# Performance work log

Hardware: AMD Instinct MI355X
Metric: run time of the kernel (lower is better)

Reference implementation:

```python
import jax, jax.numpy as jnp
import numpy as np

N = 50000
E = 1600000
HID = 128
H = 8
D = HID // H


def _layer_norm(x, g, b, eps=1e-5):
    mu = jnp.mean(x, axis=-1, keepdims=True)
    var = jnp.mean(jnp.square(x - mu), axis=-1, keepdims=True)
    return (x - mu) * jax.lax.rsqrt(var + eps) * g + b


def setup_inputs() -> dict:
    key = jax.random.key(0)
    ks = jax.random.split(key, 20)
    s = 1.0 / np.sqrt(HID)
    inp = {
        "x": jax.random.normal(ks[0], (N, HID), jnp.float32),
        "edge_index": jax.random.randint(ks[1], (2, E), 0, N, jnp.int64),
        "edge_attr": jax.random.randint(ks[2], (E,), 0, 13, jnp.int64),
        # projections (stored as [in, out] so y = x @ W + b)
        "Wq": jax.random.normal(ks[3], (HID, HID), jnp.float32) * s,
        "bq": jnp.zeros((HID,), jnp.float32),
        "Wk": jax.random.normal(ks[4], (HID, HID), jnp.float32) * s,
        "bk": jnp.zeros((HID,), jnp.float32),
        "Wv": jax.random.normal(ks[5], (HID, HID), jnp.float32) * s,
        "bv": jnp.zeros((HID,), jnp.float32),
        "Wo": jax.random.normal(ks[6], (HID, HID), jnp.float32) * s,
        "bo": jnp.zeros((HID,), jnp.float32),
        "edge_bias_table": jax.random.normal(ks[7], (13, H), jnp.float32) * 0.02,
        "W1": jax.random.normal(ks[8], (HID, 4 * HID), jnp.float32) * s,
        "b1": jnp.zeros((4 * HID,), jnp.float32),
        "W2": jax.random.normal(ks[9], (4 * HID, HID), jnp.float32) * (0.5 * s),
        "b2": jnp.zeros((HID,), jnp.float32),
        "g1": jnp.ones((HID,), jnp.float32),
        "be1": jnp.zeros((HID,), jnp.float32),
        "g2": jnp.ones((HID,), jnp.float32),
        "be2": jnp.zeros((HID,), jnp.float32),
    }
    return inp


def reference(x, edge_index, edge_attr, Wq, bq, Wk, bk, Wv, bv, Wo, bo,
              edge_bias_table, W1, b1, W2, b2, g1, be1, g2, be2):
    n = x.shape[0]
    residual = x
    h = _layer_norm(x, g1, be1)
    Q = (h @ Wq + bq).reshape(n, H, D)
    K = (h @ Wk + bk).reshape(n, H, D)
    V = (h @ Wv + bv).reshape(n, H, D)
    src, dst = edge_index[0], edge_index[1]
    # per-edge scores [E, H]
    scores = jnp.sum(Q[dst] * K[src], axis=-1) / np.sqrt(D)
    scores = scores + edge_bias_table[jnp.clip(edge_attr, 0, 12)]
    # scatter softmax over incoming edges of each dst (global max, as in source)
    scores_exp = jnp.exp(scores - jnp.max(scores))
    attn_sum = jax.ops.segment_sum(scores_exp, dst, num_segments=n)  # [N, H]
    attn_w = scores_exp / (attn_sum[dst] + 1e-8)                      # [E, H]
    messages = V[src] * attn_w[..., None]                             # [E, H, D]
    out = jax.ops.segment_sum(messages, dst, num_segments=n)          # [N, H, D]
    out = out.reshape(n, HID) @ Wo + bo
    x = residual + out  # dropout is identity in eval
    residual = x
    h2 = _layer_norm(x, g2, be2)
    ffn = jax.nn.relu(h2 @ W1 + b1) @ W2 + b2
    return residual + ffn
```

## Files before the change

### kernel.cpp

```cpp
#include <hip/hip_runtime.h>
#include <hip/hip_bf16.h>

#define N_NODES 50000
#define E_EDGES 1600000
#define HID 128
#define NH 8
#define HD 16

#define NBKT 196
#define BKT_CAP 9216
#define CHUNK_A 4096
#define EPT 16
#define BINA_BLOCKS ((E_EDGES + CHUNK_A - 1) / CHUNK_A)
#define WCVT_BLOCKS 771
#define LN_BLOCKS 12500
#define QKV_XBLOCKS ((N_NODES + 127) / 128)
#define ATTN_BLOCKS 2048

using short8 = __attribute__((ext_vector_type(8))) short;
using f32x4  = __attribute__((ext_vector_type(4))) float;
using f32x2  = __attribute__((ext_vector_type(2))) float;
typedef _Float16 h16x2 __attribute__((ext_vector_type(2)));

#if defined(__has_builtin) && __has_builtin(__builtin_amdgcn_fdot2)
#define FDOT2(a, b, c) __builtin_amdgcn_fdot2((a), (b), (c), false)
#else
__device__ __forceinline__ float FDOT2(h16x2 a, h16x2 b, float c) {
    return fmaf((float)a[0], (float)b[0], fmaf((float)a[1], (float)b[1], c));
}
#endif

__device__ __forceinline__ float wave_reduce_sum(float v) {
    #pragma unroll
    for (int off = 32; off > 0; off >>= 1) v += __shfl_xor(v, off, 64);
    return v;
}

__device__ __forceinline__ unsigned int packbf2(float a, float b) {
    __hip_bfloat162 t;
    t.x = __float2bfloat16(a);
    t.y = __float2bfloat16(b);
    unsigned int u;
    __builtin_memcpy(&u, &t, 4);
    return u;
}

__device__ __forceinline__ unsigned short bf16u(float v) {
    __hip_bfloat16 t = __float2bfloat16(v);
    unsigned short u;
    __builtin_memcpy(&u, &t, 2);
    return u;
}

__device__ __forceinline__ unsigned char fp8e(float v) {
    return (unsigned char)(__builtin_amdgcn_cvt_pk_fp8_f32(v, v, 0u, false) & 0xFFu);
}

union U4H {
    uint4 u;
    h16x2 h[4];
};

struct KV {
    U4H k0, k1;
    uint4 v;
};

__device__ __forceinline__ KV loadkv(const char* khs, const unsigned char* v8s, unsigned pk) {
    KV r;
    unsigned rr = pk & 0xFFFFu;
    r.k0.u = *(const uint4*)(khs + (rr << 8));
    r.k1.u = *(const uint4*)(khs + (rr << 8) + 16u);
    r.v = *(const uint4*)(v8s + (rr << 7));
    return r;
}

__device__ __forceinline__ void consume_kv(const KV& kv, unsigned pk, bool vd,
                                           const U4H& q0, const U4H& q1,
                                           const float* bLDS, int sub,
                                           f32x2* acc2, float& wsum) {
    float p = 0.f;
    #pragma unroll
    for (int j = 0; j < 4; ++j) p = FDOT2(q0.h[j], kv.k0.h[j], p);
    #pragma unroll
    for (int j = 0; j < 4; ++j) p = FDOT2(q1.h[j], kv.k1.h[j], p);
    float s = p + bLDS[((pk >> 16) & 0xFu) * 8 + sub];
    float w = vd ? __expf(s) : 0.f;
    wsum += w;
    f32x2 w2; w2[0] = w; w2[1] = w;
    f32x2 t;
    t = __builtin_amdgcn_cvt_pk_f32_fp8(kv.v.x, false); acc2[0] = t * w2 + acc2[0];
    t = __builtin_amdgcn_cvt_pk_f32_fp8(kv.v.x, true);  acc2[1] = t * w2 + acc2[1];
    t = __builtin_amdgcn_cvt_pk_f32_fp8(kv.v.y, false); acc2[2] = t * w2 + acc2[2];
    t = __builtin_amdgcn_cvt_pk_f32_fp8(kv.v.y, true);  acc2[3] = t * w2 + acc2[3];
    t = __builtin_amdgcn_cvt_pk_f32_fp8(kv.v.z, false); acc2[4] = t * w2 + acc2[4];
    t = __builtin_amdgcn_cvt_pk_f32_fp8(kv.v.z, true);  acc2[5] = t * w2 + acc2[5];
    t = __builtin_amdgcn_cvt_pk_f32_fp8(kv.v.w, false); acc2[6] = t * w2 + acc2[6];
    t = __builtin_amdgcn_cvt_pk_f32_fp8(kv.v.w, true);  acc2[7] = t * w2 + acc2[7];
}

__global__ __launch_bounds__(256) void prep_kernel(
    const int* __restrict__ ei, const int* __restrict__ attr,
    int* __restrict__ bcur, unsigned int* __restrict__ temp,
    const float* __restrict__ Wq, const float* __restrict__ Wk,
    const float* __restrict__ Wv, const float* __restrict__ Wo,
    const float* __restrict__ W1, const float* __restrict__ W2,
    const float* __restrict__ bq, const float* __restrict__ bk,
    const float* __restrict__ bv,
    __hip_bfloat16* __restrict__ Wqkvt, __hip_bfloat16* __restrict__ Wot,
    __hip_bfloat16* __restrict__ W1t, __hip_bfloat16* __restrict__ W2t,
    float* __restrict__ bqkv,
    const float* __restrict__ x, const float* __restrict__ g1,
    const float* __restrict__ be1, __hip_bfloat16* __restrict__ h_out) {
    __shared__ unsigned int sval[CHUNK_A];
    __shared__ unsigned short sbkt[CHUNK_A];
    __shared__ int hist[NBKT];
    __shared__ int lofs[NBKT];
    __shared__ int gbase[NBKT];
    __shared__ int lcur[NBKT];
    __shared__ int sc[256];
    const int b = blockIdx.x;
    const int tid = threadIdx.x;
    if (b < BINA_BLOCKS) {
        const int e0 = b * CHUNK_A;
        const int n = min(CHUNK_A, E_EDGES - e0);
        for (int i = tid; i < NBKT; i += 256) hist[i] = 0;
        __syncthreads();
        unsigned int v[EPT];
        short bk_[EPT];
        #pragma unroll
        for (int j = 0; j < EPT; ++j) {
            int i = tid + j * 256;
            bk_[j] = -1;
            v[j] = 0;
            if (i < n) {
                int e = e0 + i;
                int src = ei[e];
                int dst = ei[E_EDGES + e];
                int a = attr[e]; a = min(max(a, 0), 12);
                v[j] = (unsigned)src | ((unsigned)a << 16) | ((unsigned)(dst & 255) << 20);
                int bb = dst >> 8;
                bk_[j] = (short)bb;
                atomicAdd(&hist[bb], 1);
            }
        }
        __syncthreads();
        sc[tid] = (tid < NBKT) ? hist[tid] : 0;
        __syncthreads();
        for (int off = 1; off < 256; off <<= 1) {
            int xx = (tid >= off) ? sc[tid - off] : 0;
            __syncthreads();
            sc[tid] += xx;
            __syncthreads();
        }
        if (tid < NBKT) {
            int h = hist[tid];
            lofs[tid] = sc[tid] - h;
            lcur[tid] = 0;
            gbase[tid] = h ? atomicAdd(&bcur[tid], h) : 0;
        }
        __syncthreads();
        #pragma unroll
        for (int j = 0; j < EPT; ++j) {
            if (bk_[j] >= 0) {
                int p = lofs[bk_[j]] + atomicAdd(&lcur[bk_[j]], 1);
                sval[p] = v[j];
                sbkt[p] = (unsigned short)bk_[j];
            }
        }
        __syncthreads();
        for (int i = tid; i < n; i += 256) {
            int bb = sbkt[i];
            temp[(size_t)bb * BKT_CAP + gbase[bb] + (i - lofs[bb])] = sval[i];
        }
    } else if (b < BINA_BLOCKS + WCVT_BLOCKS) {
        int t = (b - BINA_BLOCKS) * 256 + tid;
        if (t >= 196608) {
            int i = t - 196608;
            if (i < 384) bqkv[i] = i < 128 ? bq[i] : (i < 256 ? bk[i - 128] : bv[i - 256]);
            return;
        }
        const float* W; __hip_bfloat16* Wt; int K, N, idx;
        if (t < 65536) {
            int which = t >> 14; idx = t & 16383; K = 128; N = 128;
            W = which == 0 ? Wq : which == 1 ? Wk : which == 2 ? Wv : Wo;
            Wt = which == 3 ? Wot : Wqkvt + which * 16384;
        } else if (t < 131072) { idx = t - 65536;  K = 128; N = 512; W = W1; Wt = W1t; }
        else                   { idx = t - 131072; K = 512; N = 128; W = W2; Wt = W2t; }
        int n = idx / K, k = idx - n * K;
        Wt[idx] = __float2bfloat16(W[(size_t)k * N + n]);
    } else {
        int wave = tid >> 6;
        int lane = tid & 63;
        int row = (b - BINA_BLOCKS - WCVT_BLOCKS) * 4 + wave;
        if (row >= N_NODES) return;
        float2 v = ((const float2*)(x + (size_t)row * HID))[lane];
        float s = wave_reduce_sum(v.x + v.y);
        float mu = s * (1.0f / HID);
        float dx = v.x - mu, dy = v.y - mu;
        float q = wave_reduce_sum(dx * dx + dy * dy);
        float rstd = rsqrtf(q * (1.0f / HID) + 1e-5f);
        float2 gg = ((const float2*)g1)[lane];
        float2 bb = ((const float2*)be1)[lane];
        __hip_bfloat162 o;
        o.x = __float2bfloat16(dx * rstd * gg.x + bb.x);
        o.y = __float2bfloat16(dy * rstd * gg.y + bb.y);
        ((__hip_bfloat162*)(h_out + (size_t)row * HID))[lane] = o;
    }
}

__global__ __launch_bounds__(512) void qkv_binb_kernel(
    const int* __restrict__ bcur, const unsigned int* __restrict__ temp,
    unsigned int* __restrict__ packed, int* __restrict__ offs,
    const __hip_bfloat16* __restrict__ A, const __hip_bfloat16* __restrict__ Wt,
    const float* __restrict__ bias,
    _Float16* __restrict__ Chh, unsigned char* __restrict__ C8, int M) {
    __shared__ short8 smem[2048 + 2048];
    const int tid = threadIdx.x;
    if (blockIdx.x < NBKT) {
        int* cnts = (int*)smem;
        int* hist = cnts + 256;
        int* cur = hist + 256;
        const int b = blockIdx.x;
        if (tid < 256) {
            cnts[tid] = (tid < NBKT) ? bcur[tid] : 0;
            hist[tid] = 0;
        }
        __syncthreads();
        for (int off = 1; off < 256; off <<= 1) {
            int x = 0;
            if (tid < 256 && tid >= off) x = cnts[tid - off];
            __syncthreads();
            if (tid < 256) cnts[tid] += x;
            __syncthreads();
        }
        const int cnt = bcur[b];
        const int start = cnts[b] - cnt;
        const size_t base = (size_t)b * BKT_CAP;
        for (int i = tid; i < cnt; i += 512)
            atomicAdd(&hist[(temp[base + i] >> 20) & 255], 1);
        __syncthreads();
        if (tid < 256) cur[tid] = hist[tid];
        __syncthreads();
        for (int off = 1; off < 256; off <<= 1) {
            int x = 0;
            if (tid < 256 && tid >= off) x = cur[tid - off];
            __syncthreads();
            if (tid < 256) cur[tid] += x;
            __syncthreads();
        }
        const int node0 = b * 256;
        if (tid < 256) {
            int excl = cur[tid] - hist[tid];
            cur[tid] = excl;
            int node = node0 + tid;
            if (node < N_NODES) offs[node] = start + excl;
        }
        if (b == NBKT - 1 && tid == 0) offs[N_NODES] = start + cnt;
        __syncthreads();
        for (int i = tid; i < cnt; i += 512) {
            unsigned int v = temp[base + i];
            int d = (v >> 20) & 255;
            int p = start + atomicAdd(&cur[d], 1);
            packed[p] = v & 0xFFFFFu;
        }
        return;
    }
    const int gb = blockIdx.x - NBKT;
    const int plane = gb / QKV_XBLOCKS;
    const int xb = gb - plane * QKV_XBLOCKS;
    const int row0 = xb * 128;
    const int col0 = plane * 128;
    const int w = tid >> 6, l = tid & 63;
    const int lr = l & 15, hi = l >> 4;
    f32x4 acc[8] = {};
    #pragma unroll
    for (int it = 0; it < 4; ++it) {
        unsigned d = tid + it * 512;
        int r = d >> 4, sd = d & 15;
        int ss = sd ^ (r & 7);
        int gr = row0 + r; if (gr >= M) gr = M - 1;
        __builtin_amdgcn_global_load_lds(
            (const __attribute__((address_space(1))) void*)(A + (size_t)gr * 128 + ss * 8),
            (__attribute__((address_space(3))) void*)(smem + (d & ~63u)),
            16, 0, 0);
    }
    #pragma unroll
    for (int it = 0; it < 4; ++it) {
        unsigned d = tid + it * 512;
        int r = d >> 4, sd = d & 15;
        int ss = sd ^ (r & 7);
        __builtin_amdgcn_global_load_lds(
            (const __attribute__((address_space(1))) void*)(Wt + (size_t)(col0 + r) * 128 + ss * 8),
            (__attribute__((address_space(3))) void*)(smem + 2048 + (d & ~63u)),
            16, 0, 0);
    }
    __syncthreads();
    const int ar = w * 16 + lr;
    #pragma unroll
    for (int ks = 0; ks < 4; ++ks) {
        int s = ks * 4 + hi;
        short8 a = smem[ar * 16 + (s ^ (ar & 7))];
        #pragma unroll
        for (int f = 0; f < 8; ++f) {
            int br = f * 16 + lr;
            short8 b = smem[2048 + br * 16 + (s ^ (br & 7))];
            acc[f] = __builtin_amdgcn_mfma_f32_16x16x32_bf16(a, b, acc[f], 0, 0, 0);
        }
    }
    const float scl = (plane == 0) ? 0.25f : 1.0f;
    #pragma unroll
    for (int f = 0; f < 8; ++f) {
        int c = col0 + f * 16 + lr;
        float bv = bias[c];
        #pragma unroll
        for (int j = 0; j < 4; ++j) {
            int r = row0 + w * 16 + hi * 4 + j;
            if (r < M) {
                float v = acc[f][j] + bv;
                if (plane < 2)
                    Chh[(size_t)plane * N_NODES * 128 + (size_t)r * 128 + (c & 127)] =
                        (_Float16)(v * scl);
                else
                    C8[(size_t)r * 128 + (c & 127)] = fp8e(v);
            }
        }
    }
}

__global__ __launch_bounds__(512) void wo_ln2_kernel(const __hip_bfloat16* __restrict__ A,
                                                     const __hip_bfloat16* __restrict__ Wt,
                                                     const float* __restrict__ bias,
                                                     const float* __restrict__ res,
                                                     __hip_bfloat16* __restrict__ Cb,
                                                     __hip_bfloat16* __restrict__ Cx,
                                                     const float* __restrict__ gw,
                                                     const float* __restrict__ bw,
                                                     int M) {
    __shared__ short8 smem[2048 + 2048];
    const int row0 = blockIdx.x * 128;
    const int tid = threadIdx.x;
    const int w = tid >> 6, l = tid & 63;
    const int lr = l & 15, hi = l >> 4;
    f32x4 acc[8] = {};
    #pragma unroll
    for (int it = 0; it < 4; ++it) {
        unsigned d = tid + it * 512;
        int r = d >> 4, sd = d & 15;
        int ss = sd ^ (r & 7);
        int gr = row0 + r; if (gr >= M) gr = M - 1;
        __builtin_amdgcn_global_load_lds(
            (const __attribute__((address_space(1))) void*)(A + (size_t)gr * 128 + ss * 8),
            (__attribute__((address_space(3))) void*)(smem + (d & ~63u)),
            16, 0, 0);
    }
    #pragma unroll
    for (int it = 0; it < 4; ++it) {
        unsigned d = tid + it * 512;
        int r = d >> 4, sd = d & 15;
        int ss = sd ^ (r & 7);
        __builtin_amdgcn_global_load_lds(
            (const __attribute__((address_space(1))) void*)(Wt + (size_t)r * 128 + ss * 8),
            (__attribute__((address_space(3))) void*)(smem + 2048 + (d & ~63u)),
            16, 0, 0);
    }
    __syncthreads();
    const int ar = w * 16 + lr;
    #pragma unroll
    for (int ks = 0; ks < 4; ++ks) {
        int s = ks * 4 + hi;
        short8 a = smem[ar * 16 + (s ^ (ar & 7))];
        #pragma unroll
        for (int f = 0; f < 8; ++f) {
            int br = f * 16 + lr;
            short8 b = smem[2048 + br * 16 + (s ^ (br & 7))];
            acc[f] = __builtin_amdgcn_mfma_f32_16x16x32_bf16(a, b, acc[f], 0, 0, 0);
        }
    }
    float vv[8][4];
    float gc[8], bc[8];
    #pragma unroll
    for (int f = 0; f < 8; ++f) {
        int c = f * 16 + lr;
        gc[f] = gw[c]; bc[f] = bw[c];
        float bv = bias[c];
        #pragma unroll
        for (int j = 0; j < 4; ++j) {
            int r = row0 + w * 16 + hi * 4 + j;
            int rr = r < M ? r : M - 1;
            vv[f][j] = acc[f][j] + bv + res[(size_t)rr * 128 + c];
        }
    }
    #pragma unroll
    for (int j = 0; j < 4; ++j) {
        int r = row0 + w * 16 + hi * 4 + j;
        float s = 0.f, qq = 0.f;
        #pragma unroll
        for (int f = 0; f < 8; ++f) { s += vv[f][j]; qq += vv[f][j] * vv[f][j]; }
        #pragma unroll
        for (int m = 1; m <= 8; m <<= 1) { s += __shfl_xor(s, m); qq += __shfl_xor(qq, m); }
        float mu = s * (1.0f / 128.0f);
        float rstd = rsqrtf(qq * (1.0f / 128.0f) - mu * mu + 1e-5f);
        if (r < M) {
            #pragma unroll
            for (int f = 0; f < 8; ++f) {
                int c = f * 16 + lr;
                Cx[(size_t)r * 128 + c] = __float2bfloat16(vv[f][j]);
                Cb[(size_t)r * 128 + c] = __float2bfloat16((vv[f][j] - mu) * rstd * gc[f] + bc[f]);
            }
        }
    }
}

__global__ __launch_bounds__(256) void ffn_fused_kernel(
    const __hip_bfloat16* __restrict__ h2,
    const __hip_bfloat16* __restrict__ W1t,
    const float* __restrict__ b1,
    const __hip_bfloat16* __restrict__ W2t,
    const float* __restrict__ b2,
    const __hip_bfloat16* __restrict__ x1b,
    float* __restrict__ outp, int M) {
    __shared__ short8 aLDS[512];
    __shared__ short8 bLDS[1024];
    __shared__ unsigned short fLDS[32 * 512];
    const int tid = threadIdx.x;
    const int row0 = blockIdx.x * 32;
    const int w = tid >> 6, l = tid & 63;
    const int lr = l & 15, hi = l >> 4;
    const int rt = w & 1, ch = w >> 1;
    #pragma unroll
    for (int it = 0; it < 2; ++it) {
        unsigned d = tid + it * 256;
        int r = d >> 4, sd = d & 15;
        int ss = sd ^ (r & 7);
        int gr = row0 + r; if (gr >= M) gr = M - 1;
        __builtin_amdgcn_global_load_lds(
            (const __attribute__((address_space(1))) void*)(h2 + (size_t)gr * 128 + ss * 8),
            (__attribute__((address_space(3))) void*)(aLDS + (d & ~63u)),
            16, 0, 0);
    }
    const int ar = rt * 16 + lr;
    for (int cc = 0; cc < 8; ++cc) {
        #pragma unroll
        for (int it = 0; it < 4; ++it) {
            unsigned d = tid + it * 256;
            int rb = d >> 4, sd = d & 15;
            int ss = sd ^ (rb & 7);
            __builtin_amdgcn_global_load_lds(
                (const __attribute__((address_space(1))) void*)(W1t + (size_t)(cc * 64 + rb) * 128 + ss * 8),
                (__attribute__((address_space(3))) void*)(bLDS + (d & ~63u)),
                16, 0, 0);
        }
        __syncthreads();
        f32x4 acc0 = {}, acc1 = {};
        #pragma unroll
        for (int ks = 0; ks < 4; ++ks) {
            int s = ks * 4 + hi;
            short8 a = aLDS[ar * 16 + (s ^ (ar & 7))];
            int rb0 = ch * 32 + lr;
            short8 b0 = bLDS[rb0 * 16 + (s ^ (rb0 & 7))];
            acc0 = __builtin_amdgcn_mfma_f32_16x16x32_bf16(a, b0, acc0, 0, 0, 0);
            int rb1 = ch * 32 + 16 + lr;
            short8 b1v = bLDS[rb1 * 16 + (s ^ (rb1 & 7))];
            acc1 = __builtin_amdgcn_mfma_f32_16x16x32_bf16(a, b1v, acc1, 0, 0, 0);
        }
        #pragma unroll
        for (int f = 0; f < 2; ++f) {
            int c = cc * 64 + ch * 32 + f * 16 + lr;
            float bv = b1[c];
            int seg = c >> 3;
            #pragma unroll
            for (int j = 0; j < 4; ++j) {
                int r = rt * 16 + hi * 4 + j;
                float v = fmaxf((f == 0 ? acc0[j] : acc1[j]) + bv, 0.f);
                fLDS[r * 512 + ((seg ^ (r & 7)) << 3) + (c & 7)] = bf16u(v);
            }
        }
        __syncthreads();
    }
    f32x4 acc2[4] = {};
    for (int kc = 0; kc < 8; ++kc) {
        #pragma unroll
        for (int it = 0; it < 4; ++it) {
            unsigned d = tid + it * 256;
            int rb = d >> 3, sd = d & 7;
            int ss = sd ^ (rb & 7);
            __builtin_amdgcn_global_load_lds(
                (const __attribute__((address_space(1))) void*)(W2t + (size_t)rb * 512 + kc * 64 + ss * 8),
                (__attribute__((address_space(3))) void*)(bLDS + (d & ~63u)),
                16, 0, 0);
        }
        __syncthreads();
        #pragma unroll
        for (int ks = 0; ks < 2; ++ks) {
            int ksg = kc * 8 + ks * 4 + hi;
            short8 a = *(const short8*)&fLDS[ar * 512 + ((ksg ^ (ar & 7)) << 3)];
            int s2 = ks * 4 + hi;
            #pragma unroll
            for (int f = 0; f < 4; ++f) {
                int rb = ch * 64 + f * 16 + lr;
                short8 b = bLDS[rb * 8 + (s2 ^ (rb & 7))];
                acc2[f] = __builtin_amdgcn_mfma_f32_16x16x32_bf16(a, b, acc2[f], 0, 0, 0);
            }
        }
        __syncthreads();
    }
    #pragma unroll
    for (int f = 0; f < 4; ++f) {
        int c = ch * 64 + f * 16 + lr;
        float bv = b2[c];
        #pragma unroll
        for (int j = 0; j < 4; ++j) {
            int r = row0 + rt * 16 + hi * 4 + j;
            if (r < M) {
                float v = acc2[f][j] + bv + __bfloat162float(x1b[(size_t)r * 128 + c]);
                outp[(size_t)r * 128 + c] = v;
            }
        }
    }
}

__global__ __launch_bounds__(256) void fused_attn_kernel(
    const unsigned int* __restrict__ packed,
    const int* __restrict__ offs,
    const _Float16* __restrict__ qkh,
    const unsigned char* __restrict__ v8p,
    const float* __restrict__ btab,
    __hip_bfloat16* __restrict__ out) {
    __shared__ float bLDS[104];
    const int tid = threadIdx.x;
    if (tid < 104) bLDS[tid] = btab[tid];
    __syncthreads();
    const int wave = tid >> 6, lane = tid & 63;
    const int slot = lane >> 3, sub = lane & 7;
    const char* qh = (const char*)qkh;
    const unsigned sb = (unsigned)sub << 5;
    const char* khs = (const char*)(qkh + (size_t)N_NODES * 128) + sb;
    const unsigned char* v8s = v8p + (sb >> 1);
    const unsigned gwave = blockIdx.x * 4 + wave;
    const unsigned stride = ATTN_BLOCKS * 4;
    for (unsigned n = gwave; n < N_NODES; n += stride) {
        U4H q0, q1;
        q0.u = *(const uint4*)(qh + (n << 8) + sb);
        q1.u = *(const uint4*)(qh + (n << 8) + sb + 16u);
        const int lo = offs[n], hi = offs[n + 1];
        const int nit = (hi - lo + 7) >> 3;
        f32x2 acc2[8] = {};
        float wsum = 0.f;
        int i = lo + slot;
        bool vd0 = i < hi;       unsigned pk0 = vd0 ? packed[i] : 0u;
        bool vd1 = i + 8 < hi;   unsigned pk1 = vd1 ? packed[i + 8] : 0u;
        KV a = loadkv(khs, v8s, pk0);
        KV b = loadkv(khs, v8s, pk1);
        int ii = i + 16;
        int rem = nit;
        while (rem >= 2) {
            const bool vd2 = ii < hi;
            const unsigned pk2 = vd2 ? packed[ii] : 0u;
            const bool vd3 = ii + 8 < hi;
            const unsigned pk3 = vd3 ? packed[ii + 8] : 0u;
            consume_kv(a, pk0, vd0, q0, q1, bLDS, sub, acc2, wsum);
            a = loadkv(khs, v8s, pk2);
            consume_kv(b, pk1, vd1, q0, q1, bLDS, sub, acc2, wsum);
            b = loadkv(khs, v8s, pk3);
            pk0 = pk2; vd0 = vd2;
            pk1 = pk3; vd1 = vd3;
            ii += 16;
            rem -= 2;
        }
        if (rem == 1) consume_kv(a, pk0, vd0, q0, q1, bLDS, sub, acc2, wsum);
        float accf[16];
        #pragma unroll
        for (int j = 0; j < 8; ++j) { accf[2 * j] = acc2[j][0]; accf[2 * j + 1] = acc2[j][1]; }
        #pragma unroll
        for (int j = 0; j < 16; ++j) {
            accf[j] += __shfl_xor(accf[j], 8);
            accf[j] += __shfl_xor(accf[j], 16);
            accf[j] += __shfl_xor(accf[j], 32);
        }
        wsum += __shfl_xor(wsum, 8);
        wsum += __shfl_xor(wsum, 16);
        wsum += __shfl_xor(wsum, 32);
        if (slot == 0) {
            float inv = 1.0f / (wsum + 1e-8f);
            uint4 o0, o1;
            o0.x = packbf2(accf[0] * inv, accf[1] * inv);
            o0.y = packbf2(accf[2] * inv, accf[3] * inv);
            o0.z = packbf2(accf[4] * inv, accf[5] * inv);
            o0.w = packbf2(accf[6] * inv, accf[7] * inv);
            o1.x = packbf2(accf[8] * inv, accf[9] * inv);
            o1.y = packbf2(accf[10] * inv, accf[11] * inv);
            o1.z = packbf2(accf[12] * inv, accf[13] * inv);
            o1.w = packbf2(accf[14] * inv, accf[15] * inv);
            char* op = (char*)out + (n << 8) + ((unsigned)sub << 5);
            *(uint4*)op = o0;
            *(uint4*)(op + 16) = o1;
        }
    }
}

extern "C" void kernel_launch(void* const* d_in, const int* in_sizes, int n_in,
                              void* d_out, int out_size, void* d_ws, size_t ws_size,
                              hipStream_t stream) {
    const float* x    = (const float*)d_in[0];
    const int*   ei   = (const int*)d_in[1];
    const int*   attr = (const int*)d_in[2];
    const float* Wq   = (const float*)d_in[3];
    const float* bq   = (const float*)d_in[4];
    const float* Wk   = (const float*)d_in[5];
    const float* bk   = (const float*)d_in[6];
    const float* Wv   = (const float*)d_in[7];
    const float* bv   = (const float*)d_in[8];
    const float* Wo   = (const float*)d_in[9];
    const float* bo   = (const float*)d_in[10];
    const float* ebt  = (const float*)d_in[11];
    const float* W1   = (const float*)d_in[12];
    const float* b1   = (const float*)d_in[13];
    const float* W2   = (const float*)d_in[14];
    const float* b2   = (const float*)d_in[15];
    const float* g1   = (const float*)d_in[16];
    const float* be1  = (const float*)d_in[17];
    const float* g2   = (const float*)d_in[18];
    const float* be2  = (const float*)d_in[19];
    float* out = (float*)d_out;

    char* ws = (char*)d_ws;
    const size_t szRowB = (size_t)N_NODES * HID * 2;
    const size_t ALIGN = 256;
    #define ALN(v) (((v) + ALIGN - 1) & ~(ALIGN - 1))
    size_t o = 0;
    __hip_bfloat16* h_buf = (__hip_bfloat16*)(ws + o); o += szRowB;
    _Float16* QKh = (_Float16*)(ws + o); o += (size_t)N_NODES * 256 * 2;
    unsigned char* V8 = (unsigned char*)(ws + o); o += (size_t)N_NODES * 128;
    unsigned int* packed = (unsigned int*)(ws + o); o += (size_t)E_EDGES * 4;
    unsigned int* temp = (unsigned int*)(ws + o); o += (size_t)NBKT * BKT_CAP * 4;
    int* bcur = (int*)(ws + o); o = ALN(o + (size_t)NBKT * 4);
    int* offs = (int*)(ws + o); o = ALN(o + (size_t)(N_NODES + 1) * 4);
    __hip_bfloat16* attn_ob = (__hip_bfloat16*)(ws + o); o += szRowB;
    __hip_bfloat16* x1b = (__hip_bfloat16*)(ws + o); o += szRowB;
    __hip_bfloat16* Wqkvt = (__hip_bfloat16*)(ws + o); o += 384 * 128 * 2;
    __hip_bfloat16* Wot = (__hip_bfloat16*)(ws + o); o += 128 * 128 * 2;
    __hip_bfloat16* W1t = (__hip_bfloat16*)(ws + o); o += 512 * 128 * 2;
    __hip_bfloat16* W2t = (__hip_bfloat16*)(ws + o); o += 128 * 512 * 2;
    float* bqkv = (float*)(ws + o); o += 384 * 4;
    __hip_bfloat16* h2 = h_buf;

    hipMemsetAsync(bcur, 0, (size_t)NBKT * 4, stream);

    prep_kernel<<<BINA_BLOCKS + WCVT_BLOCKS + LN_BLOCKS, 256, 0, stream>>>(
        ei, attr, bcur, temp,
        Wq, Wk, Wv, Wo, W1, W2, bq, bk, bv,
        Wqkvt, Wot, W1t, W2t, bqkv,
        x, g1, be1, h_buf);

    qkv_binb_kernel<<<NBKT + QKV_XBLOCKS * 3, 512, 0, stream>>>(
        bcur, temp, packed, offs,
        h_buf, Wqkvt, bqkv, QKh, V8, N_NODES);

    fused_attn_kernel<<<ATTN_BLOCKS, 256, 0, stream>>>(packed, offs, QKh, V8, ebt, attn_ob);

    wo_ln2_kernel<<<(N_NODES + 127) / 128, 512, 0, stream>>>(
        attn_ob, Wot, bo, x, h2, x1b, g2, be2, N_NODES);

    ffn_fused_kernel<<<(N_NODES + 31) / 32, 256, 0, stream>>>(
        h2, W1t, b1, W2t, b2, x1b, out, N_NODES);
}
```

Before: 208.2 us.

## Fuse Wo projection and LayerNorm2 into the FFN kernel

Merges the Wo projection + residual + LayerNorm kernel into the FFN kernel. Each 32-row block computes Wo, reduces the LN statistics across two wave groups through LDS, writes normalized h2 into LDS, and keeps the residual in fp32 registers for the final add. This removes the h2/x1b global round trip and one launch, and the residual now stays in fp32 instead of passing through bf16. In exchange every block reloads the full Wo matrix (32 KB), and LDS use per block grows.

```diff
diff --git a/kernel.cpp b/kernel.cpp
--- a/kernel.cpp
+++ b/kernel.cpp
@@ -328,101 +328,22 @@
     }
 }
 
-__global__ __launch_bounds__(512) void wo_ln2_kernel(const __hip_bfloat16* __restrict__ A,
-                                                     const __hip_bfloat16* __restrict__ Wt,
-                                                     const float* __restrict__ bias,
-                                                     const float* __restrict__ res,
-                                                     __hip_bfloat16* __restrict__ Cb,
-                                                     __hip_bfloat16* __restrict__ Cx,
-                                                     const float* __restrict__ gw,
-                                                     const float* __restrict__ bw,
-                                                     int M) {
-    __shared__ short8 smem[2048 + 2048];
-    const int row0 = blockIdx.x * 128;
-    const int tid = threadIdx.x;
-    const int w = tid >> 6, l = tid & 63;
-    const int lr = l & 15, hi = l >> 4;
-    f32x4 acc[8] = {};
-    #pragma unroll
-    for (int it = 0; it < 4; ++it) {
-        unsigned d = tid + it * 512;
-        int r = d >> 4, sd = d & 15;
-        int ss = sd ^ (r & 7);
-        int gr = row0 + r; if (gr >= M) gr = M - 1;
-        __builtin_amdgcn_global_load_lds(
-            (const __attribute__((address_space(1))) void*)(A + (size_t)gr * 128 + ss * 8),
-            (__attribute__((address_space(3))) void*)(smem + (d & ~63u)),
-            16, 0, 0);
-    }
-    #pragma unroll
-    for (int it = 0; it < 4; ++it) {
-        unsigned d = tid + it * 512;
-        int r = d >> 4, sd = d & 15;
-        int ss = sd ^ (r & 7);
-        __builtin_amdgcn_global_load_lds(
-            (const __attribute__((address_space(1))) void*)(Wt + (size_t)r * 128 + ss * 8),
-            (__attribute__((address_space(3))) void*)(smem + 2048 + (d & ~63u)),
-            16, 0, 0);
-    }
-    __syncthreads();
-    const int ar = w * 16 + lr;
-    #pragma unroll
-    for (int ks = 0; ks < 4; ++ks) {
-        int s = ks * 4 + hi;
-        short8 a = smem[ar * 16 + (s ^ (ar & 7))];
-        #pragma unroll
-        for (int f = 0; f < 8; ++f) {
-            int br = f * 16 + lr;
-            short8 b = smem[2048 + br * 16 + (s ^ (br & 7))];
-            acc[f] = __builtin_amdgcn_mfma_f32_16x16x32_bf16(a, b, acc[f], 0, 0, 0);
-        }
-    }
-    float vv[8][4];
-    float gc[8], bc[8];
-    #pragma unroll
-    for (int f = 0; f < 8; ++f) {
-        int c = f * 16 + lr;
-        gc[f] = gw[c]; bc[f] = bw[c];
-        float bv = bias[c];
-        #pragma unroll
-        for (int j = 0; j < 4; ++j) {
-            int r = row0 + w * 16 + hi * 4 + j;
-            int rr = r < M ? r : M - 1;
-            vv[f][j] = acc[f][j] + bv + res[(size_t)rr * 128 + c];
-        }
-    }
-    #pragma unroll
-    for (int j = 0; j < 4; ++j) {
-        int r = row0 + w * 16 + hi * 4 + j;
-        float s = 0.f, qq = 0.f;
-        #pragma unroll
-        for (int f = 0; f < 8; ++f) { s += vv[f][j]; qq += vv[f][j] * vv[f][j]; }
-        #pragma unroll
-        for (int m = 1; m <= 8; m <<= 1) { s += __shfl_xor(s, m); qq += __shfl_xor(qq, m); }
-        float mu = s * (1.0f / 128.0f);
-        float rstd = rsqrtf(qq * (1.0f / 128.0f) - mu * mu + 1e-5f);
-        if (r < M) {
-            #pragma unroll
-            for (int f = 0; f < 8; ++f) {
-                int c = f * 16 + lr;
-                Cx[(size_t)r * 128 + c] = __float2bfloat16(vv[f][j]);
-                Cb[(size_t)r * 128 + c] = __float2bfloat16((vv[f][j] - mu) * rstd * gc[f] + bc[f]);
-            }
-        }
-    }
-}
-
-__global__ __launch_bounds__(256) void ffn_fused_kernel(
-    const __hip_bfloat16* __restrict__ h2,
+__global__ __launch_bounds__(256) void tail_kernel(
+    const __hip_bfloat16* __restrict__ attn_ob,
+    const __hip_bfloat16* __restrict__ Wot,
+    const float* __restrict__ bo,
+    const float* __restrict__ x,
+    const float* __restrict__ g2, const float* __restrict__ be2,
     const __hip_bfloat16* __restrict__ W1t,
     const float* __restrict__ b1,
     const __hip_bfloat16* __restrict__ W2t,
     const float* __restrict__ b2,
-    const __hip_bfloat16* __restrict__ x1b,
     float* __restrict__ outp, int M) {
-    __shared__ short8 aLDS[512];
-    __shared__ short8 bLDS[1024];
-    __shared__ unsigned short fLDS[32 * 512];
+    __shared__ short8 hseg[32 * 16];
+    __shared__ short8 wseg[2048];
+    __shared__ short8 bseg[1024];
+    __shared__ float lnS[2][32];
+    __shared__ float lnQ[2][32];
     const int tid = threadIdx.x;
     const int row0 = blockIdx.x * 32;
     const int w = tid >> 6, l = tid & 63;
@@ -435,11 +356,85 @@
         int ss = sd ^ (r & 7);
         int gr = row0 + r; if (gr >= M) gr = M - 1;
         __builtin_amdgcn_global_load_lds(
-            (const __attribute__((address_space(1))) void*)(h2 + (size_t)gr * 128 + ss * 8),
-            (__attribute__((address_space(3))) void*)(aLDS + (d & ~63u)),
+            (const __attribute__((address_space(1))) void*)(attn_ob + (size_t)gr * 128 + ss * 8),
+            (__attribute__((address_space(3))) void*)(hseg + (d & ~63u)),
             16, 0, 0);
     }
+    #pragma unroll
+    for (int it = 0; it < 8; ++it) {
+        unsigned d = tid + it * 256;
+        int r = d >> 4, sd = d & 15;
+        int ss = sd ^ (r & 7);
+        __builtin_amdgcn_global_load_lds(
+            (const __attribute__((address_space(1))) void*)(Wot + (size_t)r * 128 + ss * 8),
+            (__attribute__((address_space(3))) void*)(wseg + (d & ~63u)),
+            16, 0, 0);
+    }
+    __syncthreads();
     const int ar = rt * 16 + lr;
+    f32x4 acc[4] = {};
+    #pragma unroll
+    for (int ks = 0; ks < 4; ++ks) {
+        int s = ks * 4 + hi;
+        short8 a = hseg[ar * 16 + (s ^ (ar & 7))];
+        #pragma unroll
+        for (int f = 0; f < 4; ++f) {
+            int br = ch * 64 + f * 16 + lr;
+            short8 b = wseg[br * 16 + (s ^ (br & 7))];
+            acc[f] = __builtin_amdgcn_mfma_f32_16x16x32_bf16(a, b, acc[f], 0, 0, 0);
+        }
+    }
+    float vv[4][4];
+    float gc[4], bc[4];
+    #pragma unroll
+    for (int f = 0; f < 4; ++f) {
+        int c = ch * 64 + f * 16 + lr;
+        gc[f] = g2[c]; bc[f] = be2[c];
+        float bv = bo[c];
+        #pragma unroll
+        for (int j = 0; j < 4; ++j) {
+            int r = row0 + rt * 16 + hi * 4 + j;
+            int rr = r < M ? r : M - 1;
+            vv[f][j] = acc[f][j] + bv + x[(size_t)rr * 128 + c];
+        }
+    }
+    float ps[4], pq[4];
+    #pragma unroll
+    for (int j = 0; j < 4; ++j) {
+        float s = 0.f, q = 0.f;
+        #pragma unroll
+        for (int f = 0; f < 4; ++f) { s += vv[f][j]; q += vv[f][j] * vv[f][j]; }
+        #pragma unroll
+        for (int m = 1; m <= 8; m <<= 1) { s += __shfl_xor(s, m); q += __shfl_xor(q, m); }
+        ps[j] = s; pq[j] = q;
+    }
+    if (lr == 0) {
+        #pragma unroll
+        for (int j = 0; j < 4; ++j) {
+            int r = rt * 16 + hi * 4 + j;
+            lnS[ch][r] = ps[j];
+            lnQ[ch][r] = pq[j];
+        }
+    }
+    __syncthreads();
+    unsigned short* hu = (unsigned short*)hseg;
+    #pragma unroll
+    for (int j = 0; j < 4; ++j) {
+        int r = rt * 16 + hi * 4 + j;
+        float s = lnS[0][r] + lnS[1][r];
+        float q = lnQ[0][r] + lnQ[1][r];
+        float mu = s * (1.0f / 128.0f);
+        float rstd = rsqrtf(q * (1.0f / 128.0f) - mu * mu + 1e-5f);
+        #pragma unroll
+        for (int f = 0; f < 4; ++f) {
+            int c = ch * 64 + f * 16 + lr;
+            int seg = c >> 3;
+            float hv = (vv[f][j] - mu) * rstd * gc[f] + bc[f];
+            hu[r * 128 + ((seg ^ (r & 7)) << 3) + (c & 7)] = bf16u(hv);
+        }
+    }
+    __syncthreads();
+    unsigned short* f1u = (unsigned short*)wseg;
     for (int cc = 0; cc < 8; ++cc) {
         #pragma unroll
         for (int it = 0; it < 4; ++it) {
@@ -448,21 +443,21 @@
             int ss = sd ^ (rb & 7);
             __builtin_amdgcn_global_load_lds(
                 (const __attribute__((address_space(1))) void*)(W1t + (size_t)(cc * 64 + rb) * 128 + ss * 8),
-                (__attribute__((address_space(3))) void*)(bLDS + (d & ~63u)),
+                (__attribute__((address_space(3))) void*)(bseg + (d & ~63u)),
                 16, 0, 0);
         }
         __syncthreads();
-        f32x4 acc0 = {}, acc1 = {};
+        f32x4 a0 = {}, a1 = {};
         #pragma unroll
         for (int ks = 0; ks < 4; ++ks) {
             int s = ks * 4 + hi;
-            short8 a = aLDS[ar * 16 + (s ^ (ar & 7))];
+            short8 a = hseg[ar * 16 + (s ^ (ar & 7))];
             int rb0 = ch * 32 + lr;
-            short8 b0 = bLDS[rb0 * 16 + (s ^ (rb0 & 7))];
-            acc0 = __builtin_amdgcn_mfma_f32_16x16x32_bf16(a, b0, acc0, 0, 0, 0);
+            short8 b0 = bseg[rb0 * 16 + (s ^ (rb0 & 7))];
+            a0 = __builtin_amdgcn_mfma_f32_16x16x32_bf16(a, b0, a0, 0, 0, 0);
             int rb1 = ch * 32 + 16 + lr;
-            short8 b1v = bLDS[rb1 * 16 + (s ^ (rb1 & 7))];
-            acc1 = __builtin_amdgcn_mfma_f32_16x16x32_bf16(a, b1v, acc1, 0, 0, 0);
+            short8 b1v = bseg[rb1 * 16 + (s ^ (rb1 & 7))];
+            a1 = __builtin_amdgcn_mfma_f32_16x16x32_bf16(a, b1v, a1, 0, 0, 0);
         }
         #pragma unroll
         for (int f = 0; f < 2; ++f) {
@@ -472,8 +467,8 @@
             #pragma unroll
             for (int j = 0; j < 4; ++j) {
                 int r = rt * 16 + hi * 4 + j;
-                float v = fmaxf((f == 0 ? acc0[j] : acc1[j]) + bv, 0.f);
-                fLDS[r * 512 + ((seg ^ (r & 7)) << 3) + (c & 7)] = bf16u(v);
+                float v = fmaxf((f == 0 ? a0[j] : a1[j]) + bv, 0.f);
+                f1u[r * 512 + ((seg ^ (r & 7)) << 3) + (c & 7)] = bf16u(v);
             }
         }
         __syncthreads();
@@ -487,19 +482,19 @@
             int ss = sd ^ (rb & 7);
             __builtin_amdgcn_global_load_lds(
                 (const __attribute__((address_space(1))) void*)(W2t + (size_t)rb * 512 + kc * 64 + ss * 8),
-                (__attribute__((address_space(3))) void*)(bLDS + (d & ~63u)),
+                (__attribute__((address_space(3))) void*)(bseg + (d & ~63u)),
                 16, 0, 0);
         }
         __syncthreads();
         #pragma unroll
         for (int ks = 0; ks < 2; ++ks) {
             int ksg = kc * 8 + ks * 4 + hi;
-            short8 a = *(const short8*)&fLDS[ar * 512 + ((ksg ^ (ar & 7)) << 3)];
+            short8 a = *(const short8*)&f1u[ar * 512 + ((ksg ^ (ar & 7)) << 3)];
             int s2 = ks * 4 + hi;
             #pragma unroll
             for (int f = 0; f < 4; ++f) {
                 int rb = ch * 64 + f * 16 + lr;
-                short8 b = bLDS[rb * 8 + (s2 ^ (rb & 7))];
+                short8 b = bseg[rb * 8 + (s2 ^ (rb & 7))];
                 acc2[f] = __builtin_amdgcn_mfma_f32_16x16x32_bf16(a, b, acc2[f], 0, 0, 0);
             }
         }
@@ -512,10 +507,8 @@
         #pragma unroll
         for (int j = 0; j < 4; ++j) {
             int r = row0 + rt * 16 + hi * 4 + j;
-            if (r < M) {
-                float v = acc2[f][j] + bv + __bfloat162float(x1b[(size_t)r * 128 + c]);
-                outp[(size_t)r * 128 + c] = v;
-            }
+            if (r < M)
+                outp[(size_t)r * 128 + c] = acc2[f][j] + bv + vv[f][j];
         }
     }
 }
@@ -637,13 +630,11 @@
     int* bcur = (int*)(ws + o); o = ALN(o + (size_t)NBKT * 4);
     int* offs = (int*)(ws + o); o = ALN(o + (size_t)(N_NODES + 1) * 4);
     __hip_bfloat16* attn_ob = (__hip_bfloat16*)(ws + o); o += szRowB;
-    __hip_bfloat16* x1b = (__hip_bfloat16*)(ws + o); o += szRowB;
     __hip_bfloat16* Wqkvt = (__hip_bfloat16*)(ws + o); o += 384 * 128 * 2;
     __hip_bfloat16* Wot = (__hip_bfloat16*)(ws + o); o += 128 * 128 * 2;
     __hip_bfloat16* W1t = (__hip_bfloat16*)(ws + o); o += 512 * 128 * 2;
     __hip_bfloat16* W2t = (__hip_bfloat16*)(ws + o); o += 128 * 512 * 2;
     float* bqkv = (float*)(ws + o); o += 384 * 4;
-    __hip_bfloat16* h2 = h_buf;
 
     hipMemsetAsync(bcur, 0, (size_t)NBKT * 4, stream);
 
@@ -659,9 +650,6 @@
 
     fused_attn_kernel<<<ATTN_BLOCKS, 256, 0, stream>>>(packed, offs, QKh, V8, ebt, attn_ob);
 
-    wo_ln2_kernel<<<(N_NODES + 127) / 128, 512, 0, stream>>>(
-        attn_ob, Wot, bo, x, h2, x1b, g2, be2, N_NODES);
-
-    ffn_fused_kernel<<<(N_NODES + 31) / 32, 256, 0, stream>>>(
-        h2, W1t, b1, W2t, b2, x1b, out, N_NODES);
-}
+    tail_kernel<<<(N_NODES + 31) / 32, 256, 0, stream>>>(
+        attn_ob, Wot, bo, x, g2, be2, W1t, b1, W2t, b2, out, N_NODES);
+}
```

Measured after the change: 201.1 us. -3.4%, faster.
